# Kernel optimization log

Measured on AMD Instinct MI355X. Metric: run time of the kernel, lower is better.

## Reference

```python
import jax, jax.numpy as jnp
import numpy as np

N_TOKENS = 2048
HIDDEN = 2048
N_EXPERTS = 8
TOP_K = 2
D_FF = 1408  # per-expert SwiGLU intermediate size


def setup_inputs() -> dict:
    key = jax.random.key(0)
    k_h, k_g, k_wg, k_wu, k_wd = jax.random.split(key, 5)
    s_in = 1.0 / np.sqrt(HIDDEN)
    s_ff = 1.0 / np.sqrt(D_FF)
    return {
        "h": jax.random.normal(k_h, (N_TOKENS, HIDDEN), dtype=jnp.float32),
        "gate_w": jax.random.normal(k_g, (N_EXPERTS, HIDDEN), dtype=jnp.float32) * s_in,
        "w_gate": jax.random.normal(k_wg, (N_EXPERTS, HIDDEN, D_FF), dtype=jnp.float32) * s_in,
        "w_up": jax.random.normal(k_wu, (N_EXPERTS, HIDDEN, D_FF), dtype=jnp.float32) * s_in,
        "w_down": jax.random.normal(k_wd, (N_EXPERTS, D_FF, HIDDEN), dtype=jnp.float32) * s_ff,
    }


def reference(h, gate_w, w_gate, w_up, w_down):
    # --- gate: linear (fp32) + softmax + top-k (no renorm, as in source) ---
    logits = jnp.einsum("nd,ed->ne", h.astype(jnp.float32), gate_w.astype(jnp.float32))
    scores = jax.nn.softmax(logits, axis=-1)                 # [N, E]
    topk_weight, topk_idx = jax.lax.top_k(scores, TOP_K)     # [N, K], [N, K]

    # --- per-expert SwiGLU MLP applied densely, then gather selected experts ---
    # (same math as the per-expert grouped GEMM dispatch in the eager loop)
    g = jnp.einsum("nd,edf->enf", h, w_gate)                 # [E, N, F]
    u = jnp.einsum("nd,edf->enf", h, w_up)                   # [E, N, F]
    y = jnp.einsum("enf,efd->end", jax.nn.silu(g) * u, w_down)  # [E, N, D]

    # gather each token's top-k expert outputs: [N, K, D]
    y_tok = jnp.transpose(y, (1, 0, 2))                      # [N, E, D]
    sel = jnp.take_along_axis(y_tok, topk_idx[:, :, None], axis=1)

    # weighted combine
    out = jnp.einsum("nk,nkd->nd", topk_weight.astype(h.dtype), sel)
    return out
```

## Files before the change

kernel.cpp:

```cpp
#include <hip/hip_runtime.h>
#include <hip/hip_bf16.h>
#include <stdint.h>

#define N_TOK 2048
#define HID   2048
#define NEXP  8
#define DFF   1408

typedef __attribute__((ext_vector_type(8))) short short8;
typedef __attribute__((ext_vector_type(4))) float f32x4;

__device__ __forceinline__ unsigned short f2bf(float f) {
  union { float ff; uint32_t u; } v; v.ff = f;
  return (unsigned short)((v.u + 0x7FFFu + ((v.u >> 16) & 1u)) >> 16);
}

__device__ __forceinline__ void gl2lds16(const void* g, void* l) {
  __builtin_amdgcn_global_load_lds(
      (const __attribute__((address_space(1))) void*)g,
      (__attribute__((address_space(3))) void*)l, 16, 0, 0);
}

#define MFMA16(a, b, c) __builtin_amdgcn_mfma_f32_16x16x32_bf16((a), (b), (c), 0, 0, 0)

__global__ __launch_bounds__(256) void gate_topk_k(
    const float* __restrict__ h, const float* __restrict__ gw,
    int* __restrict__ cnt, int* __restrict__ topk_idx, float* __restrict__ topk_w)
{
  int token = blockIdx.x * 4 + (threadIdx.x >> 6);
  int lane  = threadIdx.x & 63;
  const float* hr = h + (size_t)token * HID;
  float acc[NEXP];
#pragma unroll
  for (int e = 0; e < NEXP; ++e) acc[e] = 0.f;
  for (int i = lane; i < HID; i += 64) {
    float hv = hr[i];
#pragma unroll
    for (int e = 0; e < NEXP; ++e) acc[e] = fmaf(hv, gw[e * HID + i], acc[e]);
  }
#pragma unroll
  for (int e = 0; e < NEXP; ++e) {
    float a = acc[e];
#pragma unroll
    for (int s = 32; s > 0; s >>= 1) a += __shfl_xor(a, s, 64);
    acc[e] = a;
  }
  if (lane == 0) {
    float m = acc[0];
#pragma unroll
    for (int e = 1; e < NEXP; ++e) m = fmaxf(m, acc[e]);
    float w[NEXP]; float s = 0.f;
#pragma unroll
    for (int e = 0; e < NEXP; ++e) { w[e] = __expf(acc[e] - m); s += w[e]; }
    float inv = 1.f / s;
    int i0 = 0; float b0 = acc[0];
#pragma unroll
    for (int e = 1; e < NEXP; ++e) if (acc[e] > b0) { b0 = acc[e]; i0 = e; }
    int i1 = -1; float b1 = -3.4e38f;
#pragma unroll
    for (int e = 0; e < NEXP; ++e) if (e != i0 && acc[e] > b1) { b1 = acc[e]; i1 = e; }
    topk_idx[token * 2 + 0] = i0;
    topk_idx[token * 2 + 1] = i1;
    topk_w[token * 2 + 0] = w[i0] * inv;
    topk_w[token * 2 + 1] = w[i1] * inv;
    atomicAdd(&cnt[i0], 1);
    atomicAdd(&cnt[i1], 1);
  }
}

__global__ void prefix_k(const int* __restrict__ cnt, int* __restrict__ offs,
                         int* __restrict__ cursor) {
  if (threadIdx.x == 0 && blockIdx.x == 0) {
    int s = 0;
    for (int e = 0; e < NEXP; ++e) { offs[e] = s; cursor[e] = s; s += cnt[e]; }
  }
}

__global__ __launch_bounds__(256) void scatter_k(
    const int* __restrict__ topk_idx, const float* __restrict__ topk_w,
    int* __restrict__ cursor, int* __restrict__ pair_token, float* __restrict__ pair_w,
    int* __restrict__ tok_slot)
{
  int n = blockIdx.x * 256 + threadIdx.x;
  if (n >= N_TOK) return;
#pragma unroll
  for (int k = 0; k < 2; ++k) {
    int e = topk_idx[n * 2 + k];
    int p = atomicAdd(&cursor[e], 1);
    pair_token[p] = n;
    pair_w[p] = topk_w[n * 2 + k];
    tok_slot[n * 2 + k] = p;
  }
}

__global__ __launch_bounds__(256) void convert_h_k(const float* __restrict__ src,
                                                   unsigned short* __restrict__ dst) {
  int i = blockIdx.x * 256 + threadIdx.x;
  float4 a = ((const float4*)src)[(size_t)i * 2];
  float4 b = ((const float4*)src)[(size_t)i * 2 + 1];
  unsigned short o[8] = {f2bf(a.x), f2bf(a.y), f2bf(a.z), f2bf(a.w),
                         f2bf(b.x), f2bf(b.y), f2bf(b.z), f2bf(b.w)};
  *(short8*)&dst[(size_t)i * 8] = *(const short8*)o;
}

__global__ __launch_bounds__(256) void transpose_k(const float* __restrict__ s1,
                                                   unsigned short* __restrict__ d1,
                                                   const float* __restrict__ s2,
                                                   unsigned short* __restrict__ d2,
                                                   int R, int C, int nz1)
{
  __shared__ unsigned short T[64 * 66];
  const size_t sl = (size_t)R * C;
  int z = blockIdx.z;
  const float* s; unsigned short* d;
  if (z < nz1) { s = s1 + (size_t)z * sl; d = d1 + (size_t)z * sl; }
  else { s = s2 + (size_t)(z - nz1) * sl; d = d2 + (size_t)(z - nz1) * sl; }
  const int rb = blockIdx.x * 64, cb = blockIdx.y * 64;
  const int t = threadIdx.x;
  const int tr = t >> 4, tc = (t & 15) * 4;
  const float* sp = s + (size_t)(rb + tr) * C + cb + tc;
#pragma unroll
  for (int i = 0; i < 4; ++i) {
    float4 v = *(const float4*)(sp + (size_t)i * 16 * C);
    int r = tr + i * 16;
    uint32_t p0 = (uint32_t)f2bf(v.x) | ((uint32_t)f2bf(v.y) << 16);
    uint32_t p1 = (uint32_t)f2bf(v.z) | ((uint32_t)f2bf(v.w) << 16);
    *(uint32_t*)&T[r * 66 + tc]     = p0;
    *(uint32_t*)&T[r * 66 + tc + 2] = p1;
  }
  __syncthreads();
  const int f = t >> 2, ch = (t & 3) * 16;
  unsigned short* dp = d + (size_t)(cb + f) * R + rb + ch;
#pragma unroll
  for (int g = 0; g < 2; ++g) {
    unsigned short buf[8];
#pragma unroll
    for (int j = 0; j < 8; ++j) buf[j] = T[(ch + g * 8 + j) * 66 + f];
    *(short8*)(dp + g * 8) = *(const short8*)buf;
  }
}

__global__ __launch_bounds__(256) void gateup9_k(
    const unsigned short* __restrict__ hbf,
    const unsigned short* __restrict__ wgt, const unsigned short* __restrict__ wut,
    const int* __restrict__ cnt, const int* __restrict__ offs,
    const int* __restrict__ pair_token, unsigned short* __restrict__ act,
    int e_fixed, int nw, int nbcnt, size_t wstride)
{
  const int x = blockIdx.x;
  const int wti = x % nw, mb = x / nw;
  int e, nb;
  if (e_fixed >= 0) { e = e_fixed; nb = wti; }
  else { e = wti / nbcnt; nb = wti % nbcnt; }
  const int count = cnt[e];
  if (mb * 64 >= count) return;
  const int off = offs[e];
  const int rows = min(64, count - mb * 64);
  const int c0 = nb * 64;

  __shared__ unsigned short As[2][64 * 64];
  __shared__ unsigned short Bg[2][64 * 64];
  __shared__ unsigned short Bu[2][64 * 64];
  __shared__ int tok[64];

  const int t = threadIdx.x;
  if (t < 64) tok[t] = pair_token[off + mb * 64 + min(t, rows - 1)];
  __syncthreads();

  const int w = t >> 6, l = t & 63;
  const int sr = l >> 3;
  const int sc = ((l & 7) ^ sr) * 8;
  const int r0 = w * 16 + sr, r1 = w * 16 + 8 + sr;

  const size_t wb = (e_fixed >= 0) ? 0 : (size_t)e * wstride;
  const unsigned short* wgE = wgt + wb;
  const unsigned short* wuE = wut + wb;
  const unsigned short* aP0 = hbf + (size_t)tok[r0] * HID + sc;
  const unsigned short* aP1 = hbf + (size_t)tok[r1] * HID + sc;
  const unsigned short* gP0 = wgE + (size_t)(c0 + r0) * HID + sc;
  const unsigned short* gP1 = wgE + (size_t)(c0 + r1) * HID + sc;
  const unsigned short* uP0 = wuE + (size_t)(c0 + r0) * HID + sc;
  const unsigned short* uP1 = wuE + (size_t)(c0 + r1) * HID + sc;
  const int ldsLo = (w * 16) * 64, ldsHi = (w * 16 + 8) * 64;

  const int fr = l & 15, fq = l >> 4;
  const int wr = (w >> 1) * 32, wc = (w & 1) * 32;
  const int f3 = fr & 7;

  f32x4 accg[2][2], accu[2][2];
#pragma unroll
  for (int i = 0; i < 2; ++i)
#pragma unroll
    for (int j = 0; j < 2; ++j) {
      accg[i][j] = (f32x4){0.f, 0.f, 0.f, 0.f};
      accu[i][j] = (f32x4){0.f, 0.f, 0.f, 0.f};
    }

  auto stage = [&](int b, int kt) {
    gl2lds16(aP0 + kt, &As[b][ldsLo]); gl2lds16(aP1 + kt, &As[b][ldsHi]);
    gl2lds16(gP0 + kt, &Bg[b][ldsLo]); gl2lds16(gP1 + kt, &Bg[b][ldsHi]);
    gl2lds16(uP0 + kt, &Bu[b][ldsLo]); gl2lds16(uP1 + kt, &Bu[b][ldsHi]);
  };
  auto compute = [&](int b) {
    short8 af[2][2], bg[2][2], bu[2][2];
#pragma unroll
    for (int kk = 0; kk < 2; ++kk) {
      const int ch = ((kk * 4 + fq) ^ f3) * 8;
#pragma unroll
      for (int mi = 0; mi < 2; ++mi)
        af[mi][kk] = *(const short8*)&As[b][(wr + mi * 16 + fr) * 64 + ch];
#pragma unroll
      for (int ni = 0; ni < 2; ++ni) {
        bg[ni][kk] = *(const short8*)&Bg[b][(wc + ni * 16 + fr) * 64 + ch];
        bu[ni][kk] = *(const short8*)&Bu[b][(wc + ni * 16 + fr) * 64 + ch];
      }
    }
    __builtin_amdgcn_s_setprio(1);
#pragma unroll
    for (int kk = 0; kk < 2; ++kk)
#pragma unroll
      for (int mi = 0; mi < 2; ++mi)
#pragma unroll
        for (int ni = 0; ni < 2; ++ni) {
          accg[mi][ni] = MFMA16(af[mi][kk], bg[ni][kk], accg[mi][ni]);
          accu[mi][ni] = MFMA16(af[mi][kk], bu[ni][kk], accu[mi][ni]);
        }
    __builtin_amdgcn_s_setprio(0);
  };

  const int NK = HID / 64;
  stage(0, 0);
  int cur = 0;
  for (int k = 0; k + 1 < NK; ++k) {
    stage(cur ^ 1, (k + 1) * 64);
    asm volatile("s_waitcnt vmcnt(6)" ::: "memory");
    asm volatile("s_barrier" ::: "memory");
    compute(cur);
    asm volatile("s_barrier" ::: "memory");
    cur ^= 1;
  }
  asm volatile("s_waitcnt vmcnt(0)" ::: "memory");
  asm volatile("s_barrier" ::: "memory");
  compute(cur);

#pragma unroll
  for (int mi = 0; mi < 2; ++mi)
#pragma unroll
    for (int ni = 0; ni < 2; ++ni)
#pragma unroll
      for (int j = 0; j < 4; ++j) {
        int r = wr + mi * 16 + fq * 4 + j;
        if (r < rows) {
          float g = accg[mi][ni][j], u = accu[mi][ni][j];
          float a = (g / (1.f + __expf(-g))) * u;
          act[(size_t)(off + mb * 64 + r) * DFF + (c0 + wc + ni * 16 + fr)] = f2bf(a);
        }
      }
}

__global__ __launch_bounds__(256) void down9_k(
    const unsigned short* __restrict__ act, const unsigned short* __restrict__ wdt,
    const int* __restrict__ cnt, const int* __restrict__ offs,
    float* __restrict__ ypair, int e_fixed, int nw, int nbcnt, size_t wstride)
{
  const int x = blockIdx.x;
  const int wti = x % nw, mb = x / nw;
  int e, nb;
  if (e_fixed >= 0) { e = e_fixed; nb = wti; }
  else { e = wti / nbcnt; nb = wti % nbcnt; }
  const int count = cnt[e];
  if (mb * 64 >= count) return;
  const int off = offs[e];
  const int rows = min(64, count - mb * 64);
  const int c0 = nb * 128;

  __shared__ unsigned short As[2][64 * 64];
  __shared__ unsigned short Bd[2][128 * 64];

  const int t = threadIdx.x;
  const int w = t >> 6, l = t & 63;
  const int sr = l >> 3;
  const int sc = ((l & 7) ^ sr) * 8;
  const size_t wb = (e_fixed >= 0) ? 0 : (size_t)e * wstride;
  const unsigned short* wdE = wdt + wb;

  const int ra0 = min(w * 16 + sr, rows - 1), ra1 = min(w * 16 + 8 + sr, rows - 1);
  const unsigned short* aP0 = act + (size_t)(off + mb * 64 + ra0) * DFF + sc;
  const unsigned short* aP1 = act + (size_t)(off + mb * 64 + ra1) * DFF + sc;
  const int ldsALo = (w * 16) * 64, ldsAHi = (w * 16 + 8) * 64;
  const unsigned short* bP[4];
  int ldsB[4];
#pragma unroll
  for (int i = 0; i < 4; ++i) {
    int rr = w * 32 + i * 8 + sr;
    bP[i] = wdE + (size_t)(c0 + rr) * DFF + sc;
    ldsB[i] = (w * 32 + i * 8) * 64;
  }

  const int fr = l & 15, fq = l >> 4;
  const int wr = (w >> 1) * 32, wc = (w & 1) * 64;
  const int f3 = fr & 7;

  f32x4 acc[2][4];
#pragma unroll
  for (int i = 0; i < 2; ++i)
#pragma unroll
    for (int j = 0; j < 4; ++j) acc[i][j] = (f32x4){0.f, 0.f, 0.f, 0.f};

  auto stage = [&](int b, int kt) {
    gl2lds16(aP0 + kt, &As[b][ldsALo]);
    gl2lds16(aP1 + kt, &As[b][ldsAHi]);
#pragma unroll
    for (int i = 0; i < 4; ++i) gl2lds16(bP[i] + kt, &Bd[b][ldsB[i]]);
  };
  auto compute = [&](int b) {
    short8 af[2][2], bd[4][2];
#pragma unroll
    for (int kk = 0; kk < 2; ++kk) {
      const int ch = ((kk * 4 + fq) ^ f3) * 8;
#pragma unroll
      for (int mi = 0; mi < 2; ++mi)
        af[mi][kk] = *(const short8*)&As[b][(wr + mi * 16 + fr) * 64 + ch];
#pragma unroll
      for (int ni = 0; ni < 4; ++ni)
        bd[ni][kk] = *(const short8*)&Bd[b][(wc + ni * 16 + fr) * 64 + ch];
    }
    __builtin_amdgcn_s_setprio(1);
#pragma unroll
    for (int kk = 0; kk < 2; ++kk)
#pragma unroll
      for (int mi = 0; mi < 2; ++mi)
#pragma unroll
        for (int ni = 0; ni < 4; ++ni)
          acc[mi][ni] = MFMA16(af[mi][kk], bd[ni][kk], acc[mi][ni]);
    __builtin_amdgcn_s_setprio(0);
  };

  const int NK = DFF / 64;
  stage(0, 0);
  int cur = 0;
  for (int k = 0; k + 1 < NK; ++k) {
    stage(cur ^ 1, (k + 1) * 64);
    asm volatile("s_waitcnt vmcnt(6)" ::: "memory");
    asm volatile("s_barrier" ::: "memory");
    compute(cur);
    asm volatile("s_barrier" ::: "memory");
    cur ^= 1;
  }
  asm volatile("s_waitcnt vmcnt(0)" ::: "memory");
  asm volatile("s_barrier" ::: "memory");
  compute(cur);

#pragma unroll
  for (int mi = 0; mi < 2; ++mi)
#pragma unroll
    for (int ni = 0; ni < 4; ++ni)
#pragma unroll
      for (int j = 0; j < 4; ++j) {
        int r = wr + mi * 16 + fq * 4 + j;
        if (r < rows)
          ypair[(size_t)(off + mb * 64 + r) * HID + (c0 + wc + ni * 16 + fr)] = acc[mi][ni][j];
      }
}

__global__ __launch_bounds__(256) void combine_k(
    const float* __restrict__ ypair, const int* __restrict__ tok_slot,
    const float* __restrict__ topk_w, float* __restrict__ out)
{
  int i = blockIdx.x * 256 + threadIdx.x;
  int n = i >> 9;
  int dv = (i & 511) * 4;
  int s0 = tok_slot[n * 2], s1 = tok_slot[n * 2 + 1];
  float w0 = topk_w[n * 2], w1 = topk_w[n * 2 + 1];
  float4 a = *(const float4*)&ypair[(size_t)s0 * HID + dv];
  float4 b = *(const float4*)&ypair[(size_t)s1 * HID + dv];
  float4 o;
  o.x = w0 * a.x + w1 * b.x; o.y = w0 * a.y + w1 * b.y;
  o.z = w0 * a.z + w1 * b.z; o.w = w0 * a.w + w1 * b.w;
  *(float4*)&out[(size_t)n * HID + dv] = o;
}

extern "C" void kernel_launch(void* const* d_in, const int* in_sizes, int n_in,
                              void* d_out, int out_size, void* d_ws, size_t ws_size,
                              hipStream_t stream) {
  const float* h  = (const float*)d_in[0];
  const float* gw = (const float*)d_in[1];
  const float* wg = (const float*)d_in[2];
  const float* wu = (const float*)d_in[3];
  const float* wd = (const float*)d_in[4];
  float* out = (float*)d_out;

  const size_t SL = (size_t)DFF * HID;
  char* ws = (char*)d_ws;
  int*   cnt        = (int*)(ws + 0);
  int*   offs       = (int*)(ws + 32);
  int*   cursor     = (int*)(ws + 64);
  int*   pair_token = (int*)(ws + 256);
  float* pair_w     = (float*)(ws + 16640);
  int*   tok_slot   = (int*)(ws + 33024);
  int*   topk_idx   = (int*)(ws + 49408);
  float* topk_w     = (float*)(ws + 65792);
  unsigned short* act = (unsigned short*)(ws + 82176);
  unsigned short* hbf = (unsigned short*)(ws + 11616512);
  unsigned short* wgt = (unsigned short*)(ws + 20005120);
  unsigned short* wut = (unsigned short*)(ws + 66142464);
  float* ypair_full   = (float*)(ws + 66142464);
  const size_t NEED_FULL = 112279808ull;

  hipMemsetAsync(ws, 0, 256, stream);

  gate_topk_k<<<N_TOK / 4, 256, 0, stream>>>(h, gw, cnt, topk_idx, topk_w);
  prefix_k<<<1, 64, 0, stream>>>(cnt, offs, cursor);
  scatter_k<<<N_TOK / 256, 256, 0, stream>>>(topk_idx, topk_w, cursor, pair_token, pair_w, tok_slot);
  convert_h_k<<<(N_TOK * HID / 8) / 256, 256, 0, stream>>>(h, hbf);

  if (ws_size >= NEED_FULL) {
    transpose_k<<<dim3(HID / 64, DFF / 64, 16), 256, 0, stream>>>(wg, wgt, wu, wut, HID, DFF, 8);
    gateup9_k<<<176 * 16, 256, 0, stream>>>(hbf, wgt, wut, cnt, offs, pair_token, act,
                                            -1, 176, 22, SL);
    transpose_k<<<dim3(DFF / 64, HID / 64, 8), 256, 0, stream>>>(wd, wgt, wd, wgt, DFF, HID, 8);
    down9_k<<<128 * 16, 256, 0, stream>>>(act, wgt, cnt, offs, ypair_full,
                                          -1, 128, 16, SL);
    combine_k<<<(N_TOK * HID / 4) / 256, 256, 0, stream>>>(ypair_full, tok_slot, topk_w, out);
  } else {
    unsigned short* wgtE = (unsigned short*)(ws + 20005120);
    unsigned short* wutE = (unsigned short*)(ws + 25772288);
    float* ypair = (float*)(ws + 31539456);
    for (int e = 0; e < NEXP; ++e) {
      transpose_k<<<dim3(HID / 64, DFF / 64, 2), 256, 0, stream>>>(wg + e * SL, wgtE, wu + e * SL, wutE, HID, DFF, 1);
      gateup9_k<<<22 * 16, 256, 0, stream>>>(hbf, wgtE, wutE, cnt, offs, pair_token, act,
                                             e, 22, 22, 0);
    }
    for (int e = 0; e < NEXP; ++e) {
      transpose_k<<<dim3(DFF / 64, HID / 64, 1), 256, 0, stream>>>(wd + e * SL, wgtE, wd + e * SL, wgtE, DFF, HID, 1);
      down9_k<<<16 * 16, 256, 0, stream>>>(act, wgtE, cnt, offs, ypair, e, 16, 16, 0);
    }
    combine_k<<<(N_TOK * HID / 4) / 256, 256, 0, stream>>>(ypair, tok_slot, topk_w, out);
  }
}
```

Measured before the change: 319.9 us.

## Triple-buffer GEMM stages, fuse h conversion into gating, store expert outputs in bf16

Both grouped GEMM kernels move from double to triple LDS buffering, which removes the trailing barrier per k-step. The fp32-to-bf16 conversion of h is folded into the gating kernel, eliminating a separate launch and a second read of h. Expert outputs are now written in bf16 instead of fp32, halving ypair traffic in down and combine. The costs are more LDS per block (lower occupancy) and extra rounding error on the per-expert outputs.

```diff
diff --git a/kernel.cpp b/kernel.cpp
--- a/kernel.cpp
+++ b/kernel.cpp
@@ -14,6 +14,9 @@
   union { float ff; uint32_t u; } v; v.ff = f;
   return (unsigned short)((v.u + 0x7FFFu + ((v.u >> 16) & 1u)) >> 16);
 }
+__device__ __forceinline__ float bf2f(unsigned short u) {
+  union { uint32_t i; float f; } v; v.i = (uint32_t)u << 16; return v.f;
+}
 
 __device__ __forceinline__ void gl2lds16(const void* g, void* l) {
   __builtin_amdgcn_global_load_lds(
@@ -25,7 +28,8 @@
 
 __global__ __launch_bounds__(256) void gate_topk_k(
     const float* __restrict__ h, const float* __restrict__ gw,
-    int* __restrict__ cnt, int* __restrict__ topk_idx, float* __restrict__ topk_w)
+    int* __restrict__ cnt, int* __restrict__ topk_idx, float* __restrict__ topk_w,
+    unsigned short* __restrict__ hbf)
 {
   int token = blockIdx.x * 4 + (threadIdx.x >> 6);
   int lane  = threadIdx.x & 63;
@@ -33,10 +37,20 @@
   float acc[NEXP];
 #pragma unroll
   for (int e = 0; e < NEXP; ++e) acc[e] = 0.f;
-  for (int i = lane; i < HID; i += 64) {
-    float hv = hr[i];
-#pragma unroll
-    for (int e = 0; e < NEXP; ++e) acc[e] = fmaf(hv, gw[e * HID + i], acc[e]);
+  for (int c = lane * 8; c < HID; c += 512) {
+    float4 a = *(const float4*)(hr + c);
+    float4 b = *(const float4*)(hr + c + 4);
+    unsigned short o[8] = {f2bf(a.x), f2bf(a.y), f2bf(a.z), f2bf(a.w),
+                           f2bf(b.x), f2bf(b.y), f2bf(b.z), f2bf(b.w)};
+    *(short8*)&hbf[(size_t)token * HID + c] = *(const short8*)o;
+#pragma unroll
+    for (int e = 0; e < NEXP; ++e) {
+      const float* gp = gw + (size_t)e * HID + c;
+      float4 ga = *(const float4*)gp;
+      float4 gb = *(const float4*)(gp + 4);
+      acc[e] = fmaf(a.x, ga.x, fmaf(a.y, ga.y, fmaf(a.z, ga.z, fmaf(a.w, ga.w,
+               fmaf(b.x, gb.x, fmaf(b.y, gb.y, fmaf(b.z, gb.z, fmaf(b.w, gb.w, acc[e]))))))));
+    }
   }
 #pragma unroll
   for (int e = 0; e < NEXP; ++e) {
@@ -91,16 +105,6 @@
     pair_w[p] = topk_w[n * 2 + k];
     tok_slot[n * 2 + k] = p;
   }
-}
-
-__global__ __launch_bounds__(256) void convert_h_k(const float* __restrict__ src,
-                                                   unsigned short* __restrict__ dst) {
-  int i = blockIdx.x * 256 + threadIdx.x;
-  float4 a = ((const float4*)src)[(size_t)i * 2];
-  float4 b = ((const float4*)src)[(size_t)i * 2 + 1];
-  unsigned short o[8] = {f2bf(a.x), f2bf(a.y), f2bf(a.z), f2bf(a.w),
-                         f2bf(b.x), f2bf(b.y), f2bf(b.z), f2bf(b.w)};
-  *(short8*)&dst[(size_t)i * 8] = *(const short8*)o;
 }
 
 __global__ __launch_bounds__(256) void transpose_k(const float* __restrict__ s1,
@@ -140,7 +144,7 @@
   }
 }
 
-__global__ __launch_bounds__(256) void gateup9_k(
+__global__ __launch_bounds__(256) void gateup11_k(
     const unsigned short* __restrict__ hbf,
     const unsigned short* __restrict__ wgt, const unsigned short* __restrict__ wut,
     const int* __restrict__ cnt, const int* __restrict__ offs,
@@ -158,9 +162,9 @@
   const int rows = min(64, count - mb * 64);
   const int c0 = nb * 64;
 
-  __shared__ unsigned short As[2][64 * 64];
-  __shared__ unsigned short Bg[2][64 * 64];
-  __shared__ unsigned short Bu[2][64 * 64];
+  __shared__ unsigned short As[3][64 * 64];
+  __shared__ unsigned short Bg[3][64 * 64];
+  __shared__ unsigned short Bu[3][64 * 64];
   __shared__ int tok[64];
 
   const int t = threadIdx.x;
@@ -231,17 +235,18 @@
   const int NK = HID / 64;
   stage(0, 0);
   int cur = 0;
-  for (int k = 0; k + 1 < NK; ++k) {
-    stage(cur ^ 1, (k + 1) * 64);
-    asm volatile("s_waitcnt vmcnt(6)" ::: "memory");
+  for (int k = 0; k < NK; ++k) {
+    if (k + 1 < NK) {
+      int bn = cur + 1; if (bn >= 3) bn -= 3;
+      stage(bn, (k + 1) * 64);
+      asm volatile("s_waitcnt vmcnt(6)" ::: "memory");
+    } else {
+      asm volatile("s_waitcnt vmcnt(0)" ::: "memory");
+    }
     asm volatile("s_barrier" ::: "memory");
     compute(cur);
-    asm volatile("s_barrier" ::: "memory");
-    cur ^= 1;
-  }
-  asm volatile("s_waitcnt vmcnt(0)" ::: "memory");
-  asm volatile("s_barrier" ::: "memory");
-  compute(cur);
+    cur = (cur + 1 < 3) ? cur + 1 : 0;
+  }
 
 #pragma unroll
   for (int mi = 0; mi < 2; ++mi)
@@ -258,10 +263,10 @@
       }
 }
 
-__global__ __launch_bounds__(256) void down9_k(
+__global__ __launch_bounds__(256) void down11_k(
     const unsigned short* __restrict__ act, const unsigned short* __restrict__ wdt,
     const int* __restrict__ cnt, const int* __restrict__ offs,
-    float* __restrict__ ypair, int e_fixed, int nw, int nbcnt, size_t wstride)
+    unsigned short* __restrict__ ypair, int e_fixed, int nw, int nbcnt, size_t wstride)
 {
   const int x = blockIdx.x;
   const int wti = x % nw, mb = x / nw;
@@ -274,8 +279,8 @@
   const int rows = min(64, count - mb * 64);
   const int c0 = nb * 128;
 
-  __shared__ unsigned short As[2][64 * 64];
-  __shared__ unsigned short Bd[2][128 * 64];
+  __shared__ unsigned short As[3][64 * 64];
+  __shared__ unsigned short Bd[3][128 * 64];
 
   const int t = threadIdx.x;
   const int w = t >> 6, l = t & 63;
@@ -339,17 +344,18 @@
   const int NK = DFF / 64;
   stage(0, 0);
   int cur = 0;
-  for (int k = 0; k + 1 < NK; ++k) {
-    stage(cur ^ 1, (k + 1) * 64);
-    asm volatile("s_waitcnt vmcnt(6)" ::: "memory");
+  for (int k = 0; k < NK; ++k) {
+    if (k + 1 < NK) {
+      int bn = cur + 1; if (bn >= 3) bn -= 3;
+      stage(bn, (k + 1) * 64);
+      asm volatile("s_waitcnt vmcnt(6)" ::: "memory");
+    } else {
+      asm volatile("s_waitcnt vmcnt(0)" ::: "memory");
+    }
     asm volatile("s_barrier" ::: "memory");
     compute(cur);
-    asm volatile("s_barrier" ::: "memory");
-    cur ^= 1;
-  }
-  asm volatile("s_waitcnt vmcnt(0)" ::: "memory");
-  asm volatile("s_barrier" ::: "memory");
-  compute(cur);
+    cur = (cur + 1 < 3) ? cur + 1 : 0;
+  }
 
 #pragma unroll
   for (int mi = 0; mi < 2; ++mi)
@@ -359,25 +365,27 @@
       for (int j = 0; j < 4; ++j) {
         int r = wr + mi * 16 + fq * 4 + j;
         if (r < rows)
-          ypair[(size_t)(off + mb * 64 + r) * HID + (c0 + wc + ni * 16 + fr)] = acc[mi][ni][j];
+          ypair[(size_t)(off + mb * 64 + r) * HID + (c0 + wc + ni * 16 + fr)] = f2bf(acc[mi][ni][j]);
       }
 }
 
 __global__ __launch_bounds__(256) void combine_k(
-    const float* __restrict__ ypair, const int* __restrict__ tok_slot,
+    const unsigned short* __restrict__ ypair, const int* __restrict__ tok_slot,
     const float* __restrict__ topk_w, float* __restrict__ out)
 {
   int i = blockIdx.x * 256 + threadIdx.x;
-  int n = i >> 9;
-  int dv = (i & 511) * 4;
+  int n = i >> 8;
+  int dv = (i & 255) * 8;
   int s0 = tok_slot[n * 2], s1 = tok_slot[n * 2 + 1];
   float w0 = topk_w[n * 2], w1 = topk_w[n * 2 + 1];
-  float4 a = *(const float4*)&ypair[(size_t)s0 * HID + dv];
-  float4 b = *(const float4*)&ypair[(size_t)s1 * HID + dv];
-  float4 o;
-  o.x = w0 * a.x + w1 * b.x; o.y = w0 * a.y + w1 * b.y;
-  o.z = w0 * a.z + w1 * b.z; o.w = w0 * a.w + w1 * b.w;
-  *(float4*)&out[(size_t)n * HID + dv] = o;
+  short8 a = *(const short8*)&ypair[(size_t)s0 * HID + dv];
+  short8 b = *(const short8*)&ypair[(size_t)s1 * HID + dv];
+  float o[8];
+#pragma unroll
+  for (int j = 0; j < 8; ++j)
+    o[j] = w0 * bf2f((unsigned short)a[j]) + w1 * bf2f((unsigned short)b[j]);
+  *(float4*)&out[(size_t)n * HID + dv]     = *(const float4*)&o[0];
+  *(float4*)&out[(size_t)n * HID + dv + 4] = *(const float4*)&o[4];
 }
 
 extern "C" void kernel_launch(void* const* d_in, const int* in_sizes, int n_in,
@@ -404,37 +412,36 @@
   unsigned short* hbf = (unsigned short*)(ws + 11616512);
   unsigned short* wgt = (unsigned short*)(ws + 20005120);
   unsigned short* wut = (unsigned short*)(ws + 66142464);
-  float* ypair_full   = (float*)(ws + 66142464);
+  unsigned short* ypair_full = (unsigned short*)(ws + 66142464);
   const size_t NEED_FULL = 112279808ull;
 
   hipMemsetAsync(ws, 0, 256, stream);
 
-  gate_topk_k<<<N_TOK / 4, 256, 0, stream>>>(h, gw, cnt, topk_idx, topk_w);
+  gate_topk_k<<<N_TOK / 4, 256, 0, stream>>>(h, gw, cnt, topk_idx, topk_w, hbf);
   prefix_k<<<1, 64, 0, stream>>>(cnt, offs, cursor);
   scatter_k<<<N_TOK / 256, 256, 0, stream>>>(topk_idx, topk_w, cursor, pair_token, pair_w, tok_slot);
-  convert_h_k<<<(N_TOK * HID / 8) / 256, 256, 0, stream>>>(h, hbf);
 
   if (ws_size >= NEED_FULL) {
     transpose_k<<<dim3(HID / 64, DFF / 64, 16), 256, 0, stream>>>(wg, wgt, wu, wut, HID, DFF, 8);
-    gateup9_k<<<176 * 16, 256, 0, stream>>>(hbf, wgt, wut, cnt, offs, pair_token, act,
-                                            -1, 176, 22, SL);
+    gateup11_k<<<176 * 16, 256, 0, stream>>>(hbf, wgt, wut, cnt, offs, pair_token, act,
+                                             -1, 176, 22, SL);
     transpose_k<<<dim3(DFF / 64, HID / 64, 8), 256, 0, stream>>>(wd, wgt, wd, wgt, DFF, HID, 8);
-    down9_k<<<128 * 16, 256, 0, stream>>>(act, wgt, cnt, offs, ypair_full,
-                                          -1, 128, 16, SL);
-    combine_k<<<(N_TOK * HID / 4) / 256, 256, 0, stream>>>(ypair_full, tok_slot, topk_w, out);
+    down11_k<<<128 * 16, 256, 0, stream>>>(act, wgt, cnt, offs, ypair_full,
+                                           -1, 128, 16, SL);
+    combine_k<<<(N_TOK * HID / 8) / 256, 256, 0, stream>>>(ypair_full, tok_slot, topk_w, out);
   } else {
     unsigned short* wgtE = (unsigned short*)(ws + 20005120);
     unsigned short* wutE = (unsigned short*)(ws + 25772288);
-    float* ypair = (float*)(ws + 31539456);
+    unsigned short* ypair = (unsigned short*)(ws + 31539456);
     for (int e = 0; e < NEXP; ++e) {
       transpose_k<<<dim3(HID / 64, DFF / 64, 2), 256, 0, stream>>>(wg + e * SL, wgtE, wu + e * SL, wutE, HID, DFF, 1);
-      gateup9_k<<<22 * 16, 256, 0, stream>>>(hbf, wgtE, wutE, cnt, offs, pair_token, act,
-                                             e, 22, 22, 0);
+      gateup11_k<<<22 * 16, 256, 0, stream>>>(hbf, wgtE, wutE, cnt, offs, pair_token, act,
+                                              e, 22, 22, 0);
     }
     for (int e = 0; e < NEXP; ++e) {
       transpose_k<<<dim3(DFF / 64, HID / 64, 1), 256, 0, stream>>>(wd + e * SL, wgtE, wd + e * SL, wgtE, DFF, HID, 1);
-      down9_k<<<16 * 16, 256, 0, stream>>>(act, wgtE, cnt, offs, ypair, e, 16, 16, 0);
-    }
-    combine_k<<<(N_TOK * HID / 4) / 256, 256, 0, stream>>>(ypair, tok_slot, topk_w, out);
-  }
-}
+      down11_k<<<16 * 16, 256, 0, stream>>>(act, wgtE, cnt, offs, ypair, e, 16, 16, 0);
+    }
+    combine_k<<<(N_TOK * HID / 8) / 256, 256, 0, stream>>>(ypair, tok_slot, topk_w, out);
+  }
+}
```

New measurement: 322.5 us. About the same (+0.8%).
